# Kernel tuning notes

Hardware: AMD Instinct MI355X
Metric: run time of the kernel (lower is better)

The kernel has to match this reference:

```python
import jax, jax.numpy as jnp
import numpy as np

N_NODES = 100000
D = 128
N_EDGES = 640000


def setup_inputs() -> dict:
    key = jax.random.key(0)
    k1, k2, k3, k4 = jax.random.split(key, 4)
    x = jax.random.normal(k1, (N_NODES, D), dtype=jnp.float32)
    edge_index = jax.random.randint(k2, (2, N_EDGES), 0, N_NODES, dtype=jnp.int64)
    # GCNConv params: lin weight (glorot) and separate bias (zeros-init in PyG)
    W = jax.random.normal(k3, (D, D), dtype=jnp.float32) * (1.0 / np.sqrt(D))
    b = jnp.zeros((D,), dtype=jnp.float32)
    return {"x": x, "edge_index": edge_index, "W": W, "b": b}


def gcn_block(x, edge_index, W, b):
    N = x.shape[0]
    loops = jnp.arange(N, dtype=edge_index.dtype)
    src = jnp.concatenate([edge_index[0], loops])  # [E+N]
    dst = jnp.concatenate([edge_index[1], loops])  # [E+N]
    # symmetric normalization: deg over targets including self-loops
    deg = jax.ops.segment_sum(jnp.ones_like(dst, dtype=x.dtype), dst, num_segments=N)
    dinv = jnp.where(deg > 0, jax.lax.rsqrt(deg), 0.0)
    norm = dinv[src] * dinv[dst]  # [E+N]
    h = x @ W  # [N, D]
    msg = h[src] * norm[:, None]  # gather + scale: [E+N, D]
    agg = jax.ops.segment_sum(msg, dst, num_segments=N) + b  # scatter-add
    return x + jax.nn.relu(agg)  # relu + residual


def reference(x, edge_index, W, b):
    return gcn_block(x, edge_index, W, b)
```

## Files before the change

kernel.cpp:

```cpp
#include <hip/hip_runtime.h>

#define D 128
#define PAD 48

typedef __attribute__((ext_vector_type(8))) short short8;
typedef __attribute__((ext_vector_type(4))) float f32x4;

static __device__ __forceinline__ unsigned short f2bf(float f) {
    unsigned int u = __float_as_uint(f);
    u += 0x7fffu + ((u >> 16) & 1u);
    return (unsigned short)(u >> 16);
}
static __device__ __forceinline__ float bf_lo(unsigned int v) {
    return __uint_as_float(v << 16);
}
static __device__ __forceinline__ float bf_hi(unsigned int v) {
    return __uint_as_float(v & 0xffff0000u);
}

__global__ __launch_bounds__(256) void zw_k(int* __restrict__ cnt,
                                            const float* __restrict__ W,
                                            unsigned short* __restrict__ Wtg,
                                            int N1) {
    int t = threadIdx.x;
    if (blockIdx.x == gridDim.x - 1) {
        __shared__ unsigned short Wt[D * D];
        const float4* Wv = (const float4*)W;
#pragma unroll
        for (int i = 0; i < 16; ++i) {
            int idx = i * 256 + t;
            int k = idx >> 5;
            int c0 = (idx & 31) * 4;
            float4 v = Wv[idx];
            float vv[4] = {v.x, v.y, v.z, v.w};
#pragma unroll
            for (int j = 0; j < 4; ++j) {
                int c = c0 + j;
                unsigned int B = (unsigned int)c * 256 + (unsigned int)k * 2;
                unsigned int sB = B ^ (((unsigned int)c & 7u) << 4);
                *(unsigned short*)((char*)Wt + sB) = f2bf(vv[j]);
            }
        }
        __syncthreads();
        const uint4* s4 = (const uint4*)Wt;
        uint4* g4 = (uint4*)Wtg;
#pragma unroll
        for (int i = 0; i < 8; ++i) g4[i * 256 + t] = s4[i * 256 + t];
    }
    int base = blockIdx.x * 1024 + t * 4;
#pragma unroll
    for (int j = 0; j < 4; ++j)
        if (base + j < N1) cnt[base + j] = 0;
}

__global__ __launch_bounds__(256) void bg_k(const float* __restrict__ x,
                                            const unsigned short* __restrict__ Wtg,
                                            unsigned short* __restrict__ h,
                                            unsigned short* __restrict__ xb,
                                            const int* __restrict__ ei,
                                            int* __restrict__ cnt,
                                            int* __restrict__ eidxp,
                                            int2* __restrict__ spill,
                                            int N, int E, int nbin) {
    __shared__ unsigned short Wt[D * D];
    __shared__ unsigned short ost[4][16 * D];
    int t = threadIdx.x;
    int bid = (int)blockIdx.x;

    bool isbin = (bid % 3 == 2) && (bid / 3 < nbin);
    if (isbin) {
        int e = ((bid / 3) * 256 + t) * 4;
        if (e + 3 < E) {
            int4 s = *(const int4*)&ei[e];
            int4 d = *(const int4*)&ei[E + e];
            int p0 = atomicAdd(&cnt[d.x], 1);
            if (p0 < PAD) eidxp[d.x * PAD + p0] = s.x;
            else { int sp = atomicAdd(&cnt[N], 1); spill[sp] = make_int2(d.x, s.x); }
            int p1 = atomicAdd(&cnt[d.y], 1);
            if (p1 < PAD) eidxp[d.y * PAD + p1] = s.y;
            else { int sp = atomicAdd(&cnt[N], 1); spill[sp] = make_int2(d.y, s.y); }
            int p2 = atomicAdd(&cnt[d.z], 1);
            if (p2 < PAD) eidxp[d.z * PAD + p2] = s.z;
            else { int sp = atomicAdd(&cnt[N], 1); spill[sp] = make_int2(d.z, s.z); }
            int p3 = atomicAdd(&cnt[d.w], 1);
            if (p3 < PAD) eidxp[d.w * PAD + p3] = s.w;
            else { int sp = atomicAdd(&cnt[N], 1); spill[sp] = make_int2(d.w, s.w); }
        } else {
            for (int q = e; q < E; ++q) {
                int s = ei[q], d = ei[E + q];
                int p = atomicAdd(&cnt[d], 1);
                if (p < PAD) eidxp[d * PAD + p] = s;
                else { int sp = atomicAdd(&cnt[N], 1); spill[sp] = make_int2(d, s); }
            }
        }
        return;
    }

    int tile = bid - (bid / 3 < nbin ? bid / 3 : nbin);
    int w = t >> 6, l = t & 63;
    int mrow = l & 15, kgrp = l >> 4;
    int row0 = tile * 64 + w * 16;

    {
        const uint4* g4 = (const uint4*)Wtg;
        uint4* s4 = (uint4*)Wt;
#pragma unroll
        for (int i2 = 0; i2 < 8; ++i2) s4[i2 * 256 + t] = g4[i2 * 256 + t];
    }
    __syncthreads();
    if (row0 >= N) return;

    short8 a[4];
#pragma unroll
    for (int kk = 0; kk < 4; ++kk) {
        const float* p = &x[(size_t)(row0 + mrow) * D + kk * 32 + kgrp * 8];
        float4 q0 = *(const float4*)p;
        float4 q1 = *(const float4*)(p + 4);
        short8 af;
        af[0] = (short)f2bf(q0.x); af[1] = (short)f2bf(q0.y);
        af[2] = (short)f2bf(q0.z); af[3] = (short)f2bf(q0.w);
        af[4] = (short)f2bf(q1.x); af[5] = (short)f2bf(q1.y);
        af[6] = (short)f2bf(q1.z); af[7] = (short)f2bf(q1.w);
        a[kk] = af;
    }
#pragma unroll
    for (int kk = 0; kk < 4; ++kk)
        *(short8*)&xb[(size_t)(row0 + mrow) * D + kk * 32 + kgrp * 8] = a[kk];

    f32x4 acc[8];
#pragma unroll
    for (int nt = 0; nt < 8; ++nt) {
        acc[nt] = (f32x4){0.f, 0.f, 0.f, 0.f};
#pragma unroll
        for (int kk = 0; kk < 4; ++kk) {
            unsigned int c = nt * 16 + mrow;
            unsigned int B = c * 256 + (unsigned int)(kk * 32 + kgrp * 8) * 2;
            unsigned int sB = B ^ ((c & 7u) << 4);
            short8 bf = *(const short8*)((const char*)Wt + sB);
            acc[nt] = __builtin_amdgcn_mfma_f32_16x16x32_bf16(a[kk], bf, acc[nt], 0, 0, 0);
        }
    }
#pragma unroll
    for (int nt = 0; nt < 8; ++nt)
#pragma unroll
        for (int j = 0; j < 4; ++j) {
            int rr = kgrp * 4 + j;
            ost[w][rr * D + nt * 16 + mrow] = f2bf(acc[nt][j]);
        }
    {
        const uint4* os4 = (const uint4*)ost[w];
        uint4* H4 = (uint4*)h;
#pragma unroll
        for (int i2 = 0; i2 < 4; ++i2) {
            int e = i2 * 64 + l;
            H4[(size_t)row0 * 16 + e] = os4[e];
        }
    }
}

__global__ __launch_bounds__(256) void agg_k(const unsigned int* __restrict__ h2,
                                             const unsigned short* __restrict__ xb,
                                             const float* __restrict__ b,
                                             const int* __restrict__ cnt,
                                             const int* __restrict__ eidxp,
                                             const int2* __restrict__ spill,
                                             float* __restrict__ out, int N) {
    int w = threadIdx.x >> 6;
    int lane = threadIdx.x & 63;
    int g = lane >> 4;
    int col = lane & 15;
    int i0 = (blockIdx.x * 4 + w) * 4 + g;
    bool valid = i0 < N;
    int i = valid ? i0 : N - 1;

    int deg = cnt[i];
    float di = rsqrtf((float)deg + 1.0f);
    int ib = i * PAD;

    const uint4* H16 = (const uint4*)h2;

    float a0, a1, a2, a3, a4, a5, a6, a7;
    {
        uint4 sv = H16[(size_t)i * 16 + col];
        a0 = bf_lo(sv.x) * di; a1 = bf_hi(sv.x) * di;
        a2 = bf_lo(sv.y) * di; a3 = bf_hi(sv.y) * di;
        a4 = bf_lo(sv.z) * di; a5 = bf_hi(sv.z) * di;
        a6 = bf_lo(sv.w) * di; a7 = bf_hi(sv.w) * di;
    }

    int dk = deg < PAD ? deg : PAD;
    int k = 0;
    for (; k + 4 <= dk; k += 4) {
        int s0 = eidxp[ib + k];
        int s1 = eidxp[ib + k + 1];
        int s2 = eidxp[ib + k + 2];
        int s3 = eidxp[ib + k + 3];
        float e0 = rsqrtf((float)cnt[s0] + 1.0f);
        float e1 = rsqrtf((float)cnt[s1] + 1.0f);
        float e2 = rsqrtf((float)cnt[s2] + 1.0f);
        float e3 = rsqrtf((float)cnt[s3] + 1.0f);
        uint4 v0 = H16[(size_t)s0 * 16 + col];
        uint4 v1 = H16[(size_t)s1 * 16 + col];
        uint4 v2 = H16[(size_t)s2 * 16 + col];
        uint4 v3 = H16[(size_t)s3 * 16 + col];
        a0 = fmaf(bf_lo(v0.x), e0, a0); a1 = fmaf(bf_hi(v0.x), e0, a1);
        a2 = fmaf(bf_lo(v0.y), e0, a2); a3 = fmaf(bf_hi(v0.y), e0, a3);
        a4 = fmaf(bf_lo(v0.z), e0, a4); a5 = fmaf(bf_hi(v0.z), e0, a5);
        a6 = fmaf(bf_lo(v0.w), e0, a6); a7 = fmaf(bf_hi(v0.w), e0, a7);
        a0 = fmaf(bf_lo(v1.x), e1, a0); a1 = fmaf(bf_hi(v1.x), e1, a1);
        a2 = fmaf(bf_lo(v1.y), e1, a2); a3 = fmaf(bf_hi(v1.y), e1, a3);
        a4 = fmaf(bf_lo(v1.z), e1, a4); a5 = fmaf(bf_hi(v1.z), e1, a5);
        a6 = fmaf(bf_lo(v1.w), e1, a6); a7 = fmaf(bf_hi(v1.w), e1, a7);
        a0 = fmaf(bf_lo(v2.x), e2, a0); a1 = fmaf(bf_hi(v2.x), e2, a1);
        a2 = fmaf(bf_lo(v2.y), e2, a2); a3 = fmaf(bf_hi(v2.y), e2, a3);
        a4 = fmaf(bf_lo(v2.z), e2, a4); a5 = fmaf(bf_hi(v2.z), e2, a5);
        a6 = fmaf(bf_lo(v2.w), e2, a6); a7 = fmaf(bf_hi(v2.w), e2, a7);
        a0 = fmaf(bf_lo(v3.x), e3, a0); a1 = fmaf(bf_hi(v3.x), e3, a1);
        a2 = fmaf(bf_lo(v3.y), e3, a2); a3 = fmaf(bf_hi(v3.y), e3, a3);
        a4 = fmaf(bf_lo(v3.z), e3, a4); a5 = fmaf(bf_hi(v3.z), e3, a5);
        a6 = fmaf(bf_lo(v3.w), e3, a6); a7 = fmaf(bf_hi(v3.w), e3, a7);
    }
    for (; k < dk; ++k) {
        int s = eidxp[ib + k];
        float e0 = rsqrtf((float)cnt[s] + 1.0f);
        uint4 v = H16[(size_t)s * 16 + col];
        a0 = fmaf(bf_lo(v.x), e0, a0); a1 = fmaf(bf_hi(v.x), e0, a1);
        a2 = fmaf(bf_lo(v.y), e0, a2); a3 = fmaf(bf_hi(v.y), e0, a3);
        a4 = fmaf(bf_lo(v.z), e0, a4); a5 = fmaf(bf_hi(v.z), e0, a5);
        a6 = fmaf(bf_lo(v.w), e0, a6); a7 = fmaf(bf_hi(v.w), e0, a7);
    }
    if (deg > PAD) {
        int sc = cnt[N];
        for (int j = 0; j < sc; ++j) {
            int2 pr = spill[j];
            if (pr.x == i) {
                int s = pr.y;
                float e0 = rsqrtf((float)cnt[s] + 1.0f);
                uint4 v = H16[(size_t)s * 16 + col];
                a0 = fmaf(bf_lo(v.x), e0, a0); a1 = fmaf(bf_hi(v.x), e0, a1);
                a2 = fmaf(bf_lo(v.y), e0, a2); a3 = fmaf(bf_hi(v.y), e0, a3);
                a4 = fmaf(bf_lo(v.z), e0, a4); a5 = fmaf(bf_hi(v.z), e0, a5);
                a6 = fmaf(bf_lo(v.w), e0, a6); a7 = fmaf(bf_hi(v.w), e0, a7);
            }
        }
    }

    if (valid) {
        size_t ob = (size_t)i * D + col * 8;
        float4 b0 = *(const float4*)&b[col * 8];
        float4 b1 = *(const float4*)&b[col * 8 + 4];
        uint4 xv = *(const uint4*)&xb[ob];
        f32x4 o0, o1;
        o0.x = bf_lo(xv.x) + fmaxf(a0 * di + b0.x, 0.f);
        o0.y = bf_hi(xv.x) + fmaxf(a1 * di + b0.y, 0.f);
        o0.z = bf_lo(xv.y) + fmaxf(a2 * di + b0.z, 0.f);
        o0.w = bf_hi(xv.y) + fmaxf(a3 * di + b0.w, 0.f);
        o1.x = bf_lo(xv.z) + fmaxf(a4 * di + b1.x, 0.f);
        o1.y = bf_hi(xv.z) + fmaxf(a5 * di + b1.y, 0.f);
        o1.z = bf_lo(xv.w) + fmaxf(a6 * di + b1.z, 0.f);
        o1.w = bf_hi(xv.w) + fmaxf(a7 * di + b1.w, 0.f);
        __builtin_nontemporal_store(o0, (f32x4*)&out[ob]);
        __builtin_nontemporal_store(o1, (f32x4*)&out[ob + 4]);
    }
}

extern "C" void kernel_launch(void* const* d_in, const int* in_sizes, int n_in,
                              void* d_out, int out_size, void* d_ws, size_t ws_size,
                              hipStream_t stream) {
    const float* x = (const float*)d_in[0];
    const int* ei = (const int*)d_in[1];
    const float* W = (const float*)d_in[2];
    const float* b = (const float*)d_in[3];
    float* out = (float*)d_out;

    int N = in_sizes[0] / D;
    int E = in_sizes[1] / 2;

    char* ws = (char*)d_ws;
    int* cnt            = (int*)(ws + 0);
    unsigned short* Wtg = (unsigned short*)(ws + (512 << 10));
    int2* spill         = (int2*)(ws + (1024 << 10));
    int* eidxp          = (int*)(ws + (8192 << 10));
    unsigned short* h   = (unsigned short*)(ws + (28672 << 10));
    unsigned short* xb  = (unsigned short*)(ws + (55296 << 10));
    unsigned int* h2    = (unsigned int*)h;

    int N1 = N + 1;
    int nzero = (N1 + 1023) / 1024;
    zw_k<<<nzero, 256, 0, stream>>>(cnt, W, Wtg, N1);

    int ntiles = (N + 63) / 64;
    int nbin = (E / 4 + 255) / 256;
    bg_k<<<nbin + ntiles, 256, 0, stream>>>(x, Wtg, h, xb, ei, cnt, eidxp, spill,
                                            N, E, nbin);
    agg_k<<<(N + 15) / 16, 256, 0, stream>>>(h2, xb, b, cnt, eidxp, spill, out, N);
}
```

Before: 90.91 us.

## Drop bf16 x copy, process two tiles per GEMM block, widen edge binning

The GEMM kernel no longer writes a bf16 copy of x. The aggregation kernel now reads fp32 x directly with nontemporal loads for the residual, which removes a write plus a read of the intermediate but doubles the residual read bytes. Each GEMM block now handles two 64-row tiles, so the LDS load of W is amortised over twice the rows. Edge-binning threads handle 8 edges each instead of 4. The output staging buffer in LDS is now XOR-swizzled to avoid bank conflicts.

Result: slower. 93.19 us (+2.5%).

```diff
diff --git a/kernel.cpp b/kernel.cpp
--- a/kernel.cpp
+++ b/kernel.cpp
@@ -56,12 +56,11 @@
 __global__ __launch_bounds__(256) void bg_k(const float* __restrict__ x,
                                             const unsigned short* __restrict__ Wtg,
                                             unsigned short* __restrict__ h,
-                                            unsigned short* __restrict__ xb,
                                             const int* __restrict__ ei,
                                             int* __restrict__ cnt,
                                             int* __restrict__ eidxp,
                                             int2* __restrict__ spill,
-                                            int N, int E, int nbin) {
+                                            int N, int E, int nbin, int ntiles) {
     __shared__ unsigned short Wt[D * D];
     __shared__ unsigned short ost[4][16 * D];
     int t = threadIdx.x;
@@ -69,22 +68,20 @@
 
     bool isbin = (bid % 3 == 2) && (bid / 3 < nbin);
     if (isbin) {
-        int e = ((bid / 3) * 256 + t) * 4;
-        if (e + 3 < E) {
-            int4 s = *(const int4*)&ei[e];
-            int4 d = *(const int4*)&ei[E + e];
-            int p0 = atomicAdd(&cnt[d.x], 1);
-            if (p0 < PAD) eidxp[d.x * PAD + p0] = s.x;
-            else { int sp = atomicAdd(&cnt[N], 1); spill[sp] = make_int2(d.x, s.x); }
-            int p1 = atomicAdd(&cnt[d.y], 1);
-            if (p1 < PAD) eidxp[d.y * PAD + p1] = s.y;
-            else { int sp = atomicAdd(&cnt[N], 1); spill[sp] = make_int2(d.y, s.y); }
-            int p2 = atomicAdd(&cnt[d.z], 1);
-            if (p2 < PAD) eidxp[d.z * PAD + p2] = s.z;
-            else { int sp = atomicAdd(&cnt[N], 1); spill[sp] = make_int2(d.z, s.z); }
-            int p3 = atomicAdd(&cnt[d.w], 1);
-            if (p3 < PAD) eidxp[d.w * PAD + p3] = s.w;
-            else { int sp = atomicAdd(&cnt[N], 1); spill[sp] = make_int2(d.w, s.w); }
+        int e = ((bid / 3) * 256 + t) * 8;
+        if (e + 7 < E) {
+            int4 sa = *(const int4*)&ei[e];
+            int4 sb = *(const int4*)&ei[e + 4];
+            int4 da = *(const int4*)&ei[E + e];
+            int4 db = *(const int4*)&ei[E + e + 4];
+            int dd[8] = {da.x, da.y, da.z, da.w, db.x, db.y, db.z, db.w};
+            int ss[8] = {sa.x, sa.y, sa.z, sa.w, sb.x, sb.y, sb.z, sb.w};
+#pragma unroll
+            for (int j = 0; j < 8; ++j) {
+                int p = atomicAdd(&cnt[dd[j]], 1);
+                if (p < PAD) eidxp[dd[j] * PAD + p] = ss[j];
+                else { int sp = atomicAdd(&cnt[N], 1); spill[sp] = make_int2(dd[j], ss[j]); }
+            }
         } else {
             for (int q = e; q < E; ++q) {
                 int s = ei[q], d = ei[E + q];
@@ -96,10 +93,9 @@
         return;
     }
 
-    int tile = bid - (bid / 3 < nbin ? bid / 3 : nbin);
+    int tile2 = bid - (bid / 3 < nbin ? bid / 3 : nbin);
     int w = t >> 6, l = t & 63;
     int mrow = l & 15, kgrp = l >> 4;
-    int row0 = tile * 64 + w * 16;
 
     {
         const uint4* g4 = (const uint4*)Wtg;
@@ -108,58 +104,66 @@
         for (int i2 = 0; i2 < 8; ++i2) s4[i2 * 256 + t] = g4[i2 * 256 + t];
     }
     __syncthreads();
-    if (row0 >= N) return;
-
-    short8 a[4];
-#pragma unroll
-    for (int kk = 0; kk < 4; ++kk) {
-        const float* p = &x[(size_t)(row0 + mrow) * D + kk * 32 + kgrp * 8];
-        float4 q0 = *(const float4*)p;
-        float4 q1 = *(const float4*)(p + 4);
-        short8 af;
-        af[0] = (short)f2bf(q0.x); af[1] = (short)f2bf(q0.y);
-        af[2] = (short)f2bf(q0.z); af[3] = (short)f2bf(q0.w);
-        af[4] = (short)f2bf(q1.x); af[5] = (short)f2bf(q1.y);
-        af[6] = (short)f2bf(q1.z); af[7] = (short)f2bf(q1.w);
-        a[kk] = af;
-    }
-#pragma unroll
-    for (int kk = 0; kk < 4; ++kk)
-        *(short8*)&xb[(size_t)(row0 + mrow) * D + kk * 32 + kgrp * 8] = a[kk];
-
-    f32x4 acc[8];
-#pragma unroll
-    for (int nt = 0; nt < 8; ++nt) {
-        acc[nt] = (f32x4){0.f, 0.f, 0.f, 0.f};
+
+#pragma unroll
+    for (int rt = 0; rt < 2; ++rt) {
+        int tile = tile2 * 2 + rt;
+        if (tile >= ntiles) break;
+        int row0 = tile * 64 + w * 16;
+        if (row0 >= N) continue;
+
+        short8 a[4];
 #pragma unroll
         for (int kk = 0; kk < 4; ++kk) {
-            unsigned int c = nt * 16 + mrow;
-            unsigned int B = c * 256 + (unsigned int)(kk * 32 + kgrp * 8) * 2;
-            unsigned int sB = B ^ ((c & 7u) << 4);
-            short8 bf = *(const short8*)((const char*)Wt + sB);
-            acc[nt] = __builtin_amdgcn_mfma_f32_16x16x32_bf16(a[kk], bf, acc[nt], 0, 0, 0);
-        }
-    }
-#pragma unroll
-    for (int nt = 0; nt < 8; ++nt)
-#pragma unroll
-        for (int j = 0; j < 4; ++j) {
-            int rr = kgrp * 4 + j;
-            ost[w][rr * D + nt * 16 + mrow] = f2bf(acc[nt][j]);
-        }
-    {
-        const uint4* os4 = (const uint4*)ost[w];
-        uint4* H4 = (uint4*)h;
-#pragma unroll
-        for (int i2 = 0; i2 < 4; ++i2) {
-            int e = i2 * 64 + l;
-            H4[(size_t)row0 * 16 + e] = os4[e];
+            const float* p = &x[(size_t)(row0 + mrow) * D + kk * 32 + kgrp * 8];
+            float4 q0 = *(const float4*)p;
+            float4 q1 = *(const float4*)(p + 4);
+            short8 af;
+            af[0] = (short)f2bf(q0.x); af[1] = (short)f2bf(q0.y);
+            af[2] = (short)f2bf(q0.z); af[3] = (short)f2bf(q0.w);
+            af[4] = (short)f2bf(q1.x); af[5] = (short)f2bf(q1.y);
+            af[6] = (short)f2bf(q1.z); af[7] = (short)f2bf(q1.w);
+            a[kk] = af;
+        }
+
+        f32x4 acc[8];
+#pragma unroll
+        for (int nt = 0; nt < 8; ++nt) {
+            acc[nt] = (f32x4){0.f, 0.f, 0.f, 0.f};
+#pragma unroll
+            for (int kk = 0; kk < 4; ++kk) {
+                unsigned int c = nt * 16 + mrow;
+                unsigned int B = c * 256 + (unsigned int)(kk * 32 + kgrp * 8) * 2;
+                unsigned int sB = B ^ ((c & 7u) << 4);
+                short8 bf = *(const short8*)((const char*)Wt + sB);
+                acc[nt] = __builtin_amdgcn_mfma_f32_16x16x32_bf16(a[kk], bf, acc[nt], 0, 0, 0);
+            }
+        }
+#pragma unroll
+        for (int nt = 0; nt < 8; ++nt)
+#pragma unroll
+            for (int j = 0; j < 4; ++j) {
+                unsigned int rr = kgrp * 4 + j;
+                unsigned int B = rr * 256 + nt * 32 + mrow * 2;
+                unsigned int sB = B ^ ((rr & 7u) << 4);
+                *(unsigned short*)((char*)ost[w] + sB) = f2bf(acc[nt][j]);
+            }
+        {
+            const uint4* os4 = (const uint4*)ost[w];
+            uint4* H4 = (uint4*)h;
+#pragma unroll
+            for (int i2 = 0; i2 < 4; ++i2) {
+                int r2 = i2 * 4 + (l >> 4);
+                int c = l & 15;
+                uint4 v = os4[r2 * 16 + (c ^ (r2 & 7))];
+                H4[(size_t)row0 * 16 + r2 * 16 + c] = v;
+            }
         }
     }
 }
 
 __global__ __launch_bounds__(256) void agg_k(const unsigned int* __restrict__ h2,
-                                             const unsigned short* __restrict__ xb,
+                                             const float* __restrict__ x,
                                              const float* __restrict__ b,
                                              const int* __restrict__ cnt,
                                              const int* __restrict__ eidxp,
@@ -249,16 +253,19 @@
         size_t ob = (size_t)i * D + col * 8;
         float4 b0 = *(const float4*)&b[col * 8];
         float4 b1 = *(const float4*)&b[col * 8 + 4];
-        uint4 xv = *(const uint4*)&xb[ob];
+        const f32x4* px0 = (const f32x4*)&x[ob];
+        const f32x4* px1 = (const f32x4*)&x[ob + 4];
+        f32x4 x0 = __builtin_nontemporal_load(px0);
+        f32x4 x1 = __builtin_nontemporal_load(px1);
         f32x4 o0, o1;
-        o0.x = bf_lo(xv.x) + fmaxf(a0 * di + b0.x, 0.f);
-        o0.y = bf_hi(xv.x) + fmaxf(a1 * di + b0.y, 0.f);
-        o0.z = bf_lo(xv.y) + fmaxf(a2 * di + b0.z, 0.f);
-        o0.w = bf_hi(xv.y) + fmaxf(a3 * di + b0.w, 0.f);
-        o1.x = bf_lo(xv.z) + fmaxf(a4 * di + b1.x, 0.f);
-        o1.y = bf_hi(xv.z) + fmaxf(a5 * di + b1.y, 0.f);
-        o1.z = bf_lo(xv.w) + fmaxf(a6 * di + b1.z, 0.f);
-        o1.w = bf_hi(xv.w) + fmaxf(a7 * di + b1.w, 0.f);
+        o0.x = x0.x + fmaxf(a0 * di + b0.x, 0.f);
+        o0.y = x0.y + fmaxf(a1 * di + b0.y, 0.f);
+        o0.z = x0.z + fmaxf(a2 * di + b0.z, 0.f);
+        o0.w = x0.w + fmaxf(a3 * di + b0.w, 0.f);
+        o1.x = x1.x + fmaxf(a4 * di + b1.x, 0.f);
+        o1.y = x1.y + fmaxf(a5 * di + b1.y, 0.f);
+        o1.z = x1.z + fmaxf(a6 * di + b1.z, 0.f);
+        o1.w = x1.w + fmaxf(a7 * di + b1.w, 0.f);
         __builtin_nontemporal_store(o0, (f32x4*)&out[ob]);
         __builtin_nontemporal_store(o1, (f32x4*)&out[ob + 4]);
     }
@@ -282,7 +289,6 @@
     int2* spill         = (int2*)(ws + (1024 << 10));
     int* eidxp          = (int*)(ws + (8192 << 10));
     unsigned short* h   = (unsigned short*)(ws + (28672 << 10));
-    unsigned short* xb  = (unsigned short*)(ws + (55296 << 10));
     unsigned int* h2    = (unsigned int*)h;
 
     int N1 = N + 1;
@@ -290,8 +296,9 @@
     zw_k<<<nzero, 256, 0, stream>>>(cnt, W, Wtg, N1);
 
     int ntiles = (N + 63) / 64;
-    int nbin = (E / 4 + 255) / 256;
-    bg_k<<<nbin + ntiles, 256, 0, stream>>>(x, Wtg, h, xb, ei, cnt, eidxp, spill,
-                                            N, E, nbin);
-    agg_k<<<(N + 15) / 16, 256, 0, stream>>>(h2, xb, b, cnt, eidxp, spill, out, N);
-}
+    int ngt = (ntiles + 1) / 2;
+    int nbin = (E / 8 + 255) / 256;
+    bg_k<<<nbin + ngt, 256, 0, stream>>>(x, Wtg, h, ei, cnt, eidxp, spill,
+                                         N, E, nbin, ntiles);
+    agg_k<<<(N + 15) / 16, 256, 0, stream>>>(h2, x, b, cnt, eidxp, spill, out, N);
+}
```
